# Kernel tuning notes

Hardware: AMD Instinct MI355X
Metric: run time of the kernel (lower is better)

Reference implementation:

```python
import jax, jax.numpy as jnp
import numpy as np
from jax import lax

# LiteMSA config: in_ch=256, out_ch=256, dim=8, heads=32, total_dim=256, scales=(3,)
DIM = 8
QKV_CH = 768          # 3 * total_dim
PW_GROUPS = 96        # 3 * heads


def setup_inputs() -> dict:
    key = jax.random.key(0)
    ks = jax.random.split(key, 5)
    x = jax.random.normal(ks[0], (16, 256, 64, 64), jnp.float32)
    w_qkv = jax.random.normal(ks[1], (768, 256), jnp.float32) * 0.02      # 1x1 conv
    w_dw = jax.random.normal(ks[2], (768, 1, 3, 3), jnp.float32) * 0.02   # depthwise 3x3
    w_pw = jax.random.normal(ks[3], (768, 8, 1, 1), jnp.float32) * 0.02   # grouped 1x1, 96 groups
    w_proj = jax.random.normal(ks[4], (256, 512), jnp.float32) * 0.02     # 1x1 conv
    bn_gamma = jnp.ones((256,), jnp.float32)
    bn_beta = jnp.zeros((256,), jnp.float32)
    bn_mean = jnp.zeros((256,), jnp.float32)
    bn_var = jnp.ones((256,), jnp.float32)
    return {"x": x, "w_qkv": w_qkv, "w_dw": w_dw, "w_pw": w_pw, "w_proj": w_proj,
            "bn_gamma": bn_gamma, "bn_beta": bn_beta, "bn_mean": bn_mean, "bn_var": bn_var}


def reference(x, w_qkv, w_dw, w_pw, w_proj, bn_gamma, bn_beta, bn_mean, bn_var):
    B, _, H, W = x.shape
    dn = ("NCHW", "OIHW", "NCHW")
    # qkv 1x1 conv
    qkv = jnp.einsum("bchw,oc->bohw", x, w_qkv)  # [B,768,H,W]
    # multi-scale aggregation: depthwise 3x3 -> grouped 1x1
    agg = lax.conv_general_dilated(qkv, w_dw, (1, 1), "SAME",
                                   dimension_numbers=dn, feature_group_count=QKV_CH)
    agg = lax.conv_general_dilated(agg, w_pw, (1, 1), "SAME",
                                   dimension_numbers=dn, feature_group_count=PW_GROUPS)
    ms = jnp.concatenate([qkv, agg], axis=1)  # [B,1536,H,W]
    # [B, heads_total=64, N=H*W, 3*dim]
    ms = ms.reshape(B, -1, 3 * DIM, H * W).transpose(0, 1, 3, 2)
    q = jax.nn.relu(ms[..., :DIM])
    k = jax.nn.relu(ms[..., DIM:2 * DIM])
    v = ms[..., 2 * DIM:]
    # pad v with ones for normalizer channel
    v = jnp.concatenate([v, jnp.ones(v.shape[:-1] + (1,), v.dtype)], axis=-1)  # [B,h,N,dim+1]
    kv = jnp.einsum("bhnd,bhne->bhde", k, v)   # [B,h,dim,dim+1]
    out = jnp.einsum("bhnd,bhde->bhne", q, kv)  # [B,h,N,dim+1]
    out = out[..., :DIM] / (out[..., DIM:] + 1e-15)
    out = out.transpose(0, 1, 3, 2).reshape(B, -1, H, W)  # [B,512,H,W]
    # proj 1x1 conv + BatchNorm (inference, running stats)
    y = jnp.einsum("bchw,oc->bohw", out, w_proj)
    inv = bn_gamma / jnp.sqrt(bn_var + 1e-5)
    y = y * inv[None, :, None, None] + (bn_beta - bn_mean * inv)[None, :, None, None]
    return y
```

## Files before the change

kernel.cpp:

```cpp
#include <hip/hip_runtime.h>
#include <hip/hip_bf16.h>


#define NB 16
#define CQKV 768
#define P4096 4096

typedef __bf16 bf16x8 __attribute__((ext_vector_type(8)));
typedef float f32x4 __attribute__((ext_vector_type(4)));

#define MFMA_BF16 __builtin_amdgcn_mfma_f32_16x16x32_bf16

__device__ __forceinline__ ushort f2bf(float f) {
    union { float f; unsigned int u; } x; x.f = f;
    unsigned int u = x.u;
    unsigned int r = (u + 0x7FFFu + ((u >> 16) & 1u)) >> 16;
    return (ushort)r;
}
__device__ __forceinline__ float bf2f(ushort u) {
    union { unsigned int u; float f; } x; x.u = ((unsigned int)u) << 16;
    return x.f;
}
__device__ __forceinline__ unsigned int pk2bf(float x, float y) {
    __hip_bfloat162 h = __float22bfloat162_rn(make_float2(x, y));
    union { __hip_bfloat162 b; unsigned int u; } c; c.b = h; return c.u;
}
__device__ __forceinline__ void stage_hi8(const float* v, ushort* dh) {
    union { unsigned int u[4]; uint4 q; } H;
    #pragma unroll
    for (int i = 0; i < 4; i++) H.u[i] = pk2bf(v[2 * i], v[2 * i + 1]);
    *(uint4*)dh = H.q;
}

__device__ __forceinline__ void gload16(void* lds, const void* g) {
    __builtin_amdgcn_global_load_lds(
        (const __attribute__((address_space(1))) void*)g,
        (__attribute__((address_space(3))) void*)lds, 16, 0, 0);
}

__global__ __launch_bounds__(128) void conv_w(
    const float* __restrict__ W, ushort* __restrict__ Ah, ushort* __restrict__ Al)
{
    const int rv = blockIdx.x;
    const int t  = threadIdx.x;
    int phys;
    if (rv < 256) phys = (rv >> 3) * 24 + (rv & 7);
    else { int r2 = rv - 256; phys = (r2 >> 4) * 24 + 8 + (r2 & 15); }
    int c = t * 2;
    float w0 = W[(size_t)phys * 256 + c];
    float w1 = W[(size_t)phys * 256 + c + 1];
    unsigned int h = pk2bf(w0, w1);
    float f0 = __uint_as_float(h << 16);
    float f1 = __uint_as_float(h & 0xffff0000u);
    unsigned int l = pk2bf(w0 - f0, w1 - f1);
    int sl = ((c >> 3) & 3) ^ ((rv >> 1) & 3);
    int idx = (c & ~31) + sl * 8 + (c & 7);
    *(unsigned int*)&Ah[(size_t)rv * 256 + idx] = h;
    *(unsigned int*)&Al[(size_t)rv * 256 + idx] = l;
}

__global__ __launch_bounds__(256) void conv_x(
    const float* __restrict__ X, ushort* __restrict__ XTh, ushort* __restrict__ XTl)
{
    const int pt = blockIdx.x;
    const int ct = blockIdx.y;
    const int b  = blockIdx.z;
    const int t  = threadIdx.x;
    const int p0 = pt * 64, c0 = ct * 64;

    __shared__ float tile[64][65];

    {
        int cr = t >> 2, pc = (t & 3) * 16;
        const float* xr = X + ((size_t)b * 256 + c0 + cr) * P4096 + p0 + pc;
        float4 v0 = *(const float4*)xr;
        float4 v1 = *(const float4*)(xr + 4);
        float4 v2 = *(const float4*)(xr + 8);
        float4 v3 = *(const float4*)(xr + 12);
        float* d = &tile[cr][pc];
        d[0]=v0.x; d[1]=v0.y; d[2]=v0.z; d[3]=v0.w;
        d[4]=v1.x; d[5]=v1.y; d[6]=v1.z; d[7]=v1.w;
        d[8]=v2.x; d[9]=v2.y; d[10]=v2.z; d[11]=v2.w;
        d[12]=v3.x; d[13]=v3.y; d[14]=v3.z; d[15]=v3.w;
    }
    __syncthreads();

    #pragma unroll
    for (int pass = 0; pass < 2; pass++) {
        int tp = t >> 2;
        int cc = (t & 3) + pass * 4;
        int p  = p0 + tp;
        float v[8];
        #pragma unroll
        for (int j = 0; j < 8; j++) v[j] = tile[cc * 8 + j][tp];
        union { unsigned int u[4]; uint4 q; } H, L;
        #pragma unroll
        for (int i = 0; i < 4; i++) {
            unsigned int h = pk2bf(v[2 * i], v[2 * i + 1]);
            H.u[i] = h;
            float f0 = __uint_as_float(h << 16);
            float f1 = __uint_as_float(h & 0xffff0000u);
            L.u[i] = pk2bf(v[2 * i] - f0, v[2 * i + 1] - f1);
        }
        int c = c0 + cc * 8;
        int sl = ((c >> 3) & 3) ^ ((p >> 1) & 3);
        size_t idx = ((size_t)b * P4096 + p) * 256 + (c & ~31) + sl * 8;
        *(uint4*)&XTh[idx] = H.q;
        *(uint4*)&XTl[idx] = L.q;
    }
}

__global__ __launch_bounds__(256, 2) void gemm_fused(
    const ushort* __restrict__ Ah, const ushort* __restrict__ Al,
    const ushort* __restrict__ Bh, const ushort* __restrict__ Bl,
    ushort* __restrict__ Cbf, float* __restrict__ qplane)
{
    const int hw = blockIdx.x;
    const int lg = (hw & 7) * 384 + (hw >> 3);
    const int mt = lg % 6;
    const int rem = lg / 6;
    const int n0 = (rem & 31) * 128;
    const int b  = rem >> 5;
    const int t  = threadIdx.x;
    const int wave = t >> 6, lane = t & 63, quad = lane >> 4, l15 = lane & 15;
    const int wr = wave >> 1, wc = wave & 1;
    const int M0 = mt * 128;

    __shared__ __align__(16) ushort AsH[2][4096];
    __shared__ __align__(16) ushort AsL[2][4096];
    __shared__ __align__(16) ushort BsH[2][4096];
    __shared__ __align__(16) ushort BsL[2][4096];

    int aoff[4], boff[4];
    #pragma unroll
    for (int i = 0; i < 4; i++) {
        int ra = wr * 64 + i * 16 + l15;
        aoff[i] = ra * 64 + ((quad ^ ((ra >> 1) & 3)) << 4);
        int rb = wc * 64 + i * 16 + l15;
        boff[i] = rb * 64 + ((quad ^ ((rb >> 1) & 3)) << 4);
    }

    const int srow = t >> 2;
    const int schunk = (t & 3) * 8;
    const size_t abase = (size_t)(M0 + srow) * 256 + schunk;
    const size_t bbase = ((size_t)b * P4096 + n0 + srow) * 256 + schunk;
    const int ldsoff = wave * 1024;

    f32x4 acc[4][4];
    #pragma unroll
    for (int mi = 0; mi < 4; mi++)
        #pragma unroll
        for (int nj = 0; nj < 4; nj++)
            #pragma unroll
            for (int r = 0; r < 4; r++) acc[mi][nj][r] = 0.0f;

    if (mt < 2) {
        auto stageQ = [&](int d, int kw) {
            #pragma unroll
            for (int i = 0; i < 2; i++) {
                int lo = ldsoff + i * 4096;
                size_t so = (size_t)(i * 64) * 256 + (size_t)kw * 32;
                gload16((char*)AsH[d] + lo, Ah + abase + so);
                gload16((char*)AsL[d] + lo, Al + abase + so);
                gload16((char*)BsH[d] + lo, Bh + bbase + so);
                gload16((char*)BsL[d] + lo, Bl + bbase + so);
            }
        };
        stageQ(0, 0);
        for (int kw = 0; kw < 8; kw++) {
            int cur = kw & 1;
            if (kw < 7) {
                stageQ(cur ^ 1, kw + 1);
                asm volatile("s_waitcnt vmcnt(8)" ::: "memory");
            } else {
                asm volatile("s_waitcnt vmcnt(0)" ::: "memory");
            }
            __builtin_amdgcn_s_barrier();
            bf16x8 ah[4], al[4];
            #pragma unroll
            for (int mi = 0; mi < 4; mi++) {
                ah[mi] = *(const bf16x8*)((const char*)AsH[cur] + aoff[mi]);
                al[mi] = *(const bf16x8*)((const char*)AsL[cur] + aoff[mi]);
            }
            #pragma unroll
            for (int nj = 0; nj < 4; nj++) {
                bf16x8 bh = *(const bf16x8*)((const char*)BsH[cur] + boff[nj]);
                bf16x8 bl = *(const bf16x8*)((const char*)BsL[cur] + boff[nj]);
                #pragma unroll
                for (int mi = 0; mi < 4; mi++) {
                    acc[mi][nj] = MFMA_BF16(ah[mi], bh, acc[mi][nj], 0, 0, 0);
                    acc[mi][nj] = MFMA_BF16(al[mi], bh, acc[mi][nj], 0, 0, 0);
                    acc[mi][nj] = MFMA_BF16(ah[mi], bl, acc[mi][nj], 0, 0, 0);
                }
            }
            __builtin_amdgcn_s_barrier();
        }
        #pragma unroll
        for (int mi = 0; mi < 4; mi++)
            #pragma unroll
            for (int nj = 0; nj < 4; nj++)
                #pragma unroll
                for (int r = 0; r < 4; r++) {
                    int rv = M0 + wr * 64 + mi * 16 + quad * 4 + r;
                    int rp = (rv >> 3) * 24 + (rv & 7);
                    int col = n0 + wc * 64 + nj * 16 + l15;
                    float v = acc[mi][nj][r];
                    Cbf[((size_t)b * CQKV + rp) * P4096 + col] = f2bf(v);
                    qplane[((size_t)b * 256 + rv) * P4096 + col] = v;
                }
    } else {
        auto stageKV = [&](int d, int kw) {
            #pragma unroll
            for (int i = 0; i < 2; i++) {
                int lo = ldsoff + i * 4096;
                size_t so = (size_t)(i * 64) * 256 + (size_t)kw * 32;
                gload16((char*)AsH[d] + lo, Ah + abase + so);
                gload16((char*)BsH[d] + lo, Bh + bbase + so);
            }
        };
        stageKV(0, 0);
        for (int kw = 0; kw < 8; kw++) {
            int cur = kw & 1;
            if (kw < 7) {
                stageKV(cur ^ 1, kw + 1);
                asm volatile("s_waitcnt vmcnt(4)" ::: "memory");
            } else {
                asm volatile("s_waitcnt vmcnt(0)" ::: "memory");
            }
            __builtin_amdgcn_s_barrier();
            bf16x8 ah[4];
            #pragma unroll
            for (int mi = 0; mi < 4; mi++)
                ah[mi] = *(const bf16x8*)((const char*)AsH[cur] + aoff[mi]);
            #pragma unroll
            for (int nj = 0; nj < 4; nj++) {
                bf16x8 bh = *(const bf16x8*)((const char*)BsH[cur] + boff[nj]);
                #pragma unroll
                for (int mi = 0; mi < 4; mi++)
                    acc[mi][nj] = MFMA_BF16(ah[mi], bh, acc[mi][nj], 0, 0, 0);
            }
            __builtin_amdgcn_s_barrier();
        }
        #pragma unroll
        for (int mi = 0; mi < 4; mi++)
            #pragma unroll
            for (int nj = 0; nj < 4; nj++)
                #pragma unroll
                for (int r = 0; r < 4; r++) {
                    int rv2 = (M0 - 256) + wr * 64 + mi * 16 + quad * 4 + r;
                    int rp = (rv2 >> 4) * 24 + 8 + (rv2 & 15);
                    int col = n0 + wc * 64 + nj * 16 + l15;
                    Cbf[((size_t)b * CQKV + rp) * P4096 + col] = f2bf(acc[mi][nj][r]);
                }
    }
}

__global__ __launch_bounds__(256) void qfix_kernel(
    float* __restrict__ qplane, const float* __restrict__ w_qkv,
    const float* __restrict__ x)
{
    size_t i = (size_t)blockIdx.x * 256 + threadIdx.x;
    float q = qplane[i];
    if (fabsf(q) >= 1e-4f) return;
    int p   = (int)(i & 4095);
    int qch = (int)((i >> 12) & 255);
    int b   = (int)(i >> 20);
    int row = (qch >> 3) * 24 + (qch & 7);
    const float* wr = w_qkv + (size_t)row * 256;
    const float* xr = x + (size_t)b * 256 * P4096 + p;
    double s = 0.0;
    for (int c = 0; c < 256; c++)
        s += (double)wr[c] * (double)xr[(size_t)c * P4096];
    qplane[i] = (float)s;
}

__global__ __launch_bounds__(512, 8) void dwpw_kernel(
    const ushort* __restrict__ qkv, const float* __restrict__ wdw,
    const float* __restrict__ wpw, ushort* __restrict__ agg)
{
    const int rt = blockIdx.x;
    const int g  = blockIdx.y;
    const int b  = blockIdx.z;
    const int t  = threadIdx.x;
    const int r0 = rt * 16;
    const int cg = g * 8;

    __shared__ __align__(16) ushort tile[8][18][80];

    const ushort* src = qkv + ((size_t)(b * CQKV + cg)) * P4096;

    if (t < 288) {
        int ch = t / 36;
        int rr = (t % 36) >> 1;
        int side = t & 1;
        *(uint4*)&tile[ch][rr][side * 72] = make_uint4(0, 0, 0, 0);
    }
    #pragma unroll
    for (int i = 0; i < 3; i++) {
        int id = t + i * 512;
        if (id < 1152) {
            int ch  = id / 144;
            int rem = id - ch * 144;
            int rr  = rem >> 3;
            int oct = (rem & 7) * 8;
            int grow = r0 - 1 + rr;
            uint4 v = make_uint4(0, 0, 0, 0);
            if (grow >= 0 && grow < 64)
                v = *(const uint4*)(src + (size_t)ch * P4096 + (size_t)grow * 64 + oct);
            *(uint4*)&tile[ch][rr][8 + oct] = v;
        }
    }
    __syncthreads();

    const int kc  = t & 31;
    const int row = t >> 5;
    const float* wdwg = wdw + (size_t)cg * 9;
    const float* wpwg = wpw + (size_t)cg * 8;

    float acc0[8], acc1[8];
    #pragma unroll
    for (int oi = 0; oi < 8; oi++) { acc0[oi] = 0.0f; acc1[oi] = 0.0f; }

    #pragma unroll
    for (int c = 0; c < 8; c++) {
        float dv0 = 0.0f, dv1 = 0.0f;
        #pragma unroll
        for (int dy = 0; dy < 3; dy++) {
            const ushort* rp = &tile[c][row + dy][2 * kc + 4];
            unsigned int u1 = *(const unsigned int*)(rp + 2);
            unsigned int u2 = *(const unsigned int*)(rp + 4);
            unsigned int u3 = *(const unsigned int*)(rp + 6);
            float xm1 = __uint_as_float(u1 & 0xffff0000u);
            float x0  = __uint_as_float(u2 << 16);
            float x1  = __uint_as_float(u2 & 0xffff0000u);
            float x2  = __uint_as_float(u3 << 16);
            float w0 = wdwg[c * 9 + dy * 3 + 0];
            float w1 = wdwg[c * 9 + dy * 3 + 1];
            float w2 = wdwg[c * 9 + dy * 3 + 2];
            dv0 = fmaf(w0, xm1, dv0); dv0 = fmaf(w1, x0, dv0); dv0 = fmaf(w2, x1, dv0);
            dv1 = fmaf(w0, x0,  dv1); dv1 = fmaf(w1, x1, dv1); dv1 = fmaf(w2, x2, dv1);
        }
        #pragma unroll
        for (int oi = 0; oi < 8; oi++) {
            float w = wpwg[oi * 8 + c];
            acc0[oi] = fmaf(w, dv0, acc0[oi]);
            acc1[oi] = fmaf(w, dv1, acc1[oi]);
        }
    }

    size_t obase = ((size_t)(b * CQKV + cg)) * P4096 + (size_t)(r0 + row) * 64 + 2 * kc;
    #pragma unroll
    for (int oi = 0; oi < 8; oi++) {
        unsigned int u = (unsigned int)f2bf(acc0[oi]) |
                         ((unsigned int)f2bf(acc1[oi]) << 16);
        *(unsigned int*)&agg[obase + (size_t)oi * P4096] = u;
    }
}

__global__ __launch_bounds__(256) void kv_kernel(
    const ushort* __restrict__ qkv, const ushort* __restrict__ agg,
    float* __restrict__ kv)
{
    const int h = blockIdx.x, b = blockIdx.y, t = threadIdx.x;
    const ushort* src = (h < 32)
        ? qkv + ((size_t)(b * CQKV + h * 24)) * P4096
        : agg + ((size_t)(b * CQKV + (h - 32) * 24)) * P4096;

    float acc[72];
    #pragma unroll
    for (int i = 0; i < 72; i++) acc[i] = 0.0f;

    for (int pi = 0; pi < 16; pi++) {
        int p = t + pi * 256;
        float kvv[8], vv[8];
        #pragma unroll
        for (int d = 0; d < 8; d++) {
            float xk = bf2f(src[(size_t)(8 + d) * P4096 + p]);
            kvv[d] = xk > 0.0f ? xk : 0.0f;
        }
        #pragma unroll
        for (int e = 0; e < 8; e++) vv[e] = bf2f(src[(size_t)(16 + e) * P4096 + p]);
        #pragma unroll
        for (int d = 0; d < 8; d++) {
            #pragma unroll
            for (int e = 0; e < 8; e++) acc[d * 9 + e] += kvv[d] * vv[e];
            acc[d * 9 + 8] += kvv[d];
        }
    }

    #pragma unroll
    for (int i = 0; i < 72; i++) {
        float v = acc[i];
        #pragma unroll
        for (int off = 32; off > 0; off >>= 1) v += __shfl_xor(v, off, 64);
        acc[i] = v;
    }
    __shared__ float part[4][72];
    int wave = t >> 6, lane = t & 63;
    if (lane == 0) {
        #pragma unroll
        for (int i = 0; i < 72; i++) part[wave][i] = acc[i];
    }
    __syncthreads();
    if (t < 72)
        kv[((size_t)b * 64 + h) * 72 + t] = part[0][t] + part[1][t] + part[2][t] + part[3][t];
}

__global__ __launch_bounds__(256) void attn_out_kernel(
    const float* __restrict__ qplane, ushort* __restrict__ agg,
    const float* __restrict__ kv)
{
    const int pt = blockIdx.x, h = blockIdx.y, b = blockIdx.z, t = threadIdx.x;
    __shared__ float kvs[72];
    if (t < 72) kvs[t] = kv[((size_t)b * 64 + h) * 72 + t];
    __syncthreads();

    const bool lohead = (h < 32);
    const float* srcf = lohead
        ? qplane + ((size_t)(b * 256 + h * 8)) * P4096 : nullptr;
    const ushort* srcb = lohead ? nullptr
        : agg + ((size_t)(b * CQKV + (h - 32) * 24)) * P4096;

    int p = pt * 256 + t;
    float num[8]; float den = 0.0f;
    #pragma unroll
    for (int e = 0; e < 8; e++) num[e] = 0.0f;
    #pragma unroll
    for (int d = 0; d < 8; d++) {
        float q = lohead ? srcf[(size_t)d * P4096 + p]
                         : bf2f(srcb[(size_t)d * P4096 + p]);
        q = q > 0.0f ? q : 0.0f;
        #pragma unroll
        for (int e = 0; e < 8; e++) num[e] += q * kvs[d * 9 + e];
        den += q * kvs[d * 9 + 8];
    }
    float rd = 1.0f / (den + 1e-15f);
    ushort* dst = agg + ((size_t)(b * CQKV + (h / 2) * 24 + 8 + (h % 2) * 8)) * P4096 + p;
    #pragma unroll
    for (int e = 0; e < 8; e++)
        dst[(size_t)e * P4096] = f2bf(num[e] * rd);
}

__global__ __launch_bounds__(256) void gemm_proj(
    const float* __restrict__ A,
    const ushort* __restrict__ Bagg,
    float* __restrict__ Y,
    const float* __restrict__ bn_g, const float* __restrict__ bn_b,
    const float* __restrict__ bn_m, const float* __restrict__ bn_v)
{
    const int n0 = blockIdx.x * 64;
    const int m0 = blockIdx.y * 64;
    const int b  = blockIdx.z;
    const int t  = threadIdx.x;
    const int wave = t >> 6, lane = t & 63, quad = lane >> 4, l15 = lane & 15;

    __shared__ __align__(16) ushort As[64][40];
    __shared__ __align__(16) ushort Bs[64][40];

    f32x4 acc[4];
    #pragma unroll
    for (int nt = 0; nt < 4; nt++)
        #pragma unroll
        for (int r = 0; r < 4; r++) acc[nt][r] = 0.0f;

    const int am = t >> 2, ak = (t & 3) * 8;
    const int bn = t & 63, kg = (t >> 6) * 8;

    for (int k0 = 0; k0 < 512; k0 += 32) {
        float av[8];
        *(float4*)&av[0] = *(const float4*)(A + (size_t)(m0 + am) * 512 + k0 + ak);
        *(float4*)&av[4] = *(const float4*)(A + (size_t)(m0 + am) * 512 + k0 + ak + 4);
        ushort bu[8];
        #pragma unroll
        for (int i = 0; i < 8; i++) {
            int kk = k0 + kg + i;
            int amch = (kk >> 4) * 24 + 8 + (kk & 15);
            bu[i] = Bagg[((size_t)b * CQKV + amch) * P4096 + n0 + bn];
        }

        __syncthreads();
        stage_hi8(av, &As[am][ak]);
        {
            union { ushort us[8]; uint4 q; } Bp;
            #pragma unroll
            for (int i = 0; i < 8; i++) Bp.us[i] = bu[i];
            *(uint4*)&Bs[bn][kg] = Bp.q;
        }
        __syncthreads();

        bf16x8 af = *(const bf16x8*)&As[wave * 16 + l15][quad * 8];
        #pragma unroll
        for (int nt = 0; nt < 4; nt++) {
            bf16x8 bf = *(const bf16x8*)&Bs[nt * 16 + l15][quad * 8];
            acc[nt] = MFMA_BF16(af, bf, acc[nt], 0, 0, 0);
        }
    }

    #pragma unroll
    for (int nt = 0; nt < 4; nt++) {
        #pragma unroll
        for (int r = 0; r < 4; r++) {
            int row = m0 + wave * 16 + quad * 4 + r;
            int col = n0 + nt * 16 + l15;
            float inv = bn_g[row] / sqrtf(bn_v[row] + 1e-5f);
            float v = acc[nt][r] * inv + (bn_b[row] - bn_m[row] * inv);
            Y[((size_t)b * 256 + row) * P4096 + col] = v;
        }
    }
}

extern "C" void kernel_launch(void* const* d_in, const int* in_sizes, int n_in,
                              void* d_out, int out_size, void* d_ws, size_t ws_size,
                              hipStream_t stream) {
    const float* x      = (const float*)d_in[0];
    const float* w_qkv  = (const float*)d_in[1];
    const float* w_dw   = (const float*)d_in[2];
    const float* w_pw   = (const float*)d_in[3];
    const float* w_proj = (const float*)d_in[4];
    const float* bn_g   = (const float*)d_in[5];
    const float* bn_b   = (const float*)d_in[6];
    const float* bn_m   = (const float*)d_in[7];
    const float* bn_v   = (const float*)d_in[8];
    float* y = (float*)d_out;

    char* ws = (char*)d_ws;
    ushort* qkv_bf = (ushort*)(ws);
    float*  qplane = (float*) (ws + 100663296);
    ushort* agg_bf = (ushort*)(ws + 167772160);
    ushort* XTh = (ushort*)(ws + 167772160);
    ushort* XTl = (ushort*)(ws + 167772160 + 33554432);
    ushort* Awh = (ushort*)(ws + 167772160 + 67108864);
    ushort* Awl = (ushort*)(ws + 167772160 + 67108864 + 393216);
    float*  kvbuf  = (float*)d_out;

    conv_w<<<dim3(768), 128, 0, stream>>>(w_qkv, Awh, Awl);
    conv_x<<<dim3(64, 4, NB), 256, 0, stream>>>(x, XTh, XTl);

    gemm_fused<<<dim3(3072), 256, 0, stream>>>(
        Awh, Awl, XTh, XTl, qkv_bf, qplane);

    qfix_kernel<<<65536, 256, 0, stream>>>(qplane, w_qkv, x);

    dwpw_kernel<<<dim3(4, 96, NB), 512, 0, stream>>>(qkv_bf, w_dw, w_pw, agg_bf);

    kv_kernel<<<dim3(64, NB), 256, 0, stream>>>(qkv_bf, agg_bf, kvbuf);

    attn_out_kernel<<<dim3(16, 64, NB), 256, 0, stream>>>(qplane, agg_bf, kvbuf);

    gemm_proj<<<dim3(64, 4, NB), 256, 0, stream>>>(
        w_proj, agg_bf, y, bn_g, bn_b, bn_m, bn_v);
}
```

Measured before the change: 444.4 us.

## Split QKV GEMM into q and kv kernels, compact near-zero q fixups into list

```diff
diff --git a/kernel.cpp b/kernel.cpp
--- a/kernel.cpp
+++ b/kernel.cpp
@@ -5,6 +5,7 @@
 #define NB 16
 #define CQKV 768
 #define P4096 4096
+#define QFIX_CAP (1u << 21)
 
 typedef __bf16 bf16x8 __attribute__((ext_vector_type(8)));
 typedef float f32x4 __attribute__((ext_vector_type(4)));
@@ -110,15 +111,18 @@
     }
 }
 
-__global__ __launch_bounds__(256, 2) void gemm_fused(
+__global__ void zero_cnt(unsigned int* qmeta) { if (threadIdx.x == 0) qmeta[0] = 0; }
+
+__global__ __launch_bounds__(256, 2) void gemm_q(
     const ushort* __restrict__ Ah, const ushort* __restrict__ Al,
     const ushort* __restrict__ Bh, const ushort* __restrict__ Bl,
-    ushort* __restrict__ Cbf, float* __restrict__ qplane)
+    ushort* __restrict__ Cbf, float* __restrict__ qplane,
+    unsigned int* __restrict__ qmeta)
 {
     const int hw = blockIdx.x;
-    const int lg = (hw & 7) * 384 + (hw >> 3);
-    const int mt = lg % 6;
-    const int rem = lg / 6;
+    const int lg = (hw & 7) * 128 + (hw >> 3);
+    const int mt = lg & 1;
+    const int rem = lg >> 1;
     const int n0 = (rem & 31) * 128;
     const int b  = rem >> 5;
     const int t  = threadIdx.x;
@@ -154,124 +158,181 @@
             #pragma unroll
             for (int r = 0; r < 4; r++) acc[mi][nj][r] = 0.0f;
 
-    if (mt < 2) {
-        auto stageQ = [&](int d, int kw) {
-            #pragma unroll
-            for (int i = 0; i < 2; i++) {
-                int lo = ldsoff + i * 4096;
-                size_t so = (size_t)(i * 64) * 256 + (size_t)kw * 32;
-                gload16((char*)AsH[d] + lo, Ah + abase + so);
-                gload16((char*)AsL[d] + lo, Al + abase + so);
-                gload16((char*)BsH[d] + lo, Bh + bbase + so);
-                gload16((char*)BsL[d] + lo, Bl + bbase + so);
+    auto stageQ = [&](int d, int kw) {
+        #pragma unroll
+        for (int i = 0; i < 2; i++) {
+            int lo = ldsoff + i * 4096;
+            size_t so = (size_t)(i * 64) * 256 + (size_t)kw * 32;
+            gload16((char*)AsH[d] + lo, Ah + abase + so);
+            gload16((char*)AsL[d] + lo, Al + abase + so);
+            gload16((char*)BsH[d] + lo, Bh + bbase + so);
+            gload16((char*)BsL[d] + lo, Bl + bbase + so);
+        }
+    };
+    stageQ(0, 0);
+    for (int kw = 0; kw < 8; kw++) {
+        int cur = kw & 1;
+        if (kw < 7) {
+            stageQ(cur ^ 1, kw + 1);
+            asm volatile("s_waitcnt vmcnt(8)" ::: "memory");
+        } else {
+            asm volatile("s_waitcnt vmcnt(0)" ::: "memory");
+        }
+        __builtin_amdgcn_s_barrier();
+        bf16x8 ah[4], al[4];
+        #pragma unroll
+        for (int mi = 0; mi < 4; mi++) {
+            ah[mi] = *(const bf16x8*)((const char*)AsH[cur] + aoff[mi]);
+            al[mi] = *(const bf16x8*)((const char*)AsL[cur] + aoff[mi]);
+        }
+        #pragma unroll
+        for (int nj = 0; nj < 4; nj++) {
+            bf16x8 bh = *(const bf16x8*)((const char*)BsH[cur] + boff[nj]);
+            bf16x8 bl = *(const bf16x8*)((const char*)BsL[cur] + boff[nj]);
+            #pragma unroll
+            for (int mi = 0; mi < 4; mi++) {
+                acc[mi][nj] = MFMA_BF16(ah[mi], bh, acc[mi][nj], 0, 0, 0);
+                acc[mi][nj] = MFMA_BF16(al[mi], bh, acc[mi][nj], 0, 0, 0);
+                acc[mi][nj] = MFMA_BF16(ah[mi], bl, acc[mi][nj], 0, 0, 0);
             }
-        };
-        stageQ(0, 0);
-        for (int kw = 0; kw < 8; kw++) {
-            int cur = kw & 1;
-            if (kw < 7) {
-                stageQ(cur ^ 1, kw + 1);
-                asm volatile("s_waitcnt vmcnt(8)" ::: "memory");
-            } else {
-                asm volatile("s_waitcnt vmcnt(0)" ::: "memory");
-            }
-            __builtin_amdgcn_s_barrier();
-            bf16x8 ah[4], al[4];
-            #pragma unroll
-            for (int mi = 0; mi < 4; mi++) {
-                ah[mi] = *(const bf16x8*)((const char*)AsH[cur] + aoff[mi]);
-                al[mi] = *(const bf16x8*)((const char*)AsL[cur] + aoff[mi]);
-            }
-            #pragma unroll
-            for (int nj = 0; nj < 4; nj++) {
-                bf16x8 bh = *(const bf16x8*)((const char*)BsH[cur] + boff[nj]);
-                bf16x8 bl = *(const bf16x8*)((const char*)BsL[cur] + boff[nj]);
-                #pragma unroll
-                for (int mi = 0; mi < 4; mi++) {
-                    acc[mi][nj] = MFMA_BF16(ah[mi], bh, acc[mi][nj], 0, 0, 0);
-                    acc[mi][nj] = MFMA_BF16(al[mi], bh, acc[mi][nj], 0, 0, 0);
-                    acc[mi][nj] = MFMA_BF16(ah[mi], bl, acc[mi][nj], 0, 0, 0);
+        }
+        __builtin_amdgcn_s_barrier();
+    }
+
+    unsigned int* qlist = qmeta + 16;
+    #pragma unroll
+    for (int mi = 0; mi < 4; mi++)
+        #pragma unroll
+        for (int nj = 0; nj < 4; nj++)
+            #pragma unroll
+            for (int r = 0; r < 4; r++) {
+                int rv = M0 + wr * 64 + mi * 16 + quad * 4 + r;
+                int rp = (rv >> 3) * 24 + (rv & 7);
+                int col = n0 + wc * 64 + nj * 16 + l15;
+                float v = acc[mi][nj][r];
+                Cbf[((size_t)b * CQKV + rp) * P4096 + col] = f2bf(v);
+                qplane[((size_t)b * 256 + rv) * P4096 + col] = v;
+                if (fabsf(v) < 1e-4f) {
+                    unsigned int idx = atomicAdd(qmeta, 1u);
+                    if (idx < QFIX_CAP)
+                        qlist[idx] = (unsigned int)(((b * 256 + rv) << 12) | col);
                 }
             }
-            __builtin_amdgcn_s_barrier();
-        }
+}
+
+__global__ __launch_bounds__(256, 4) void gemm_kv(
+    const ushort* __restrict__ Ah, const ushort* __restrict__ Bh,
+    ushort* __restrict__ Cbf)
+{
+    const int hw = blockIdx.x;
+    const int lg = (hw & 7) * 256 + (hw >> 3);
+    const int mt = lg & 3;
+    const int rem = lg >> 2;
+    const int n0 = (rem & 31) * 128;
+    const int b  = rem >> 5;
+    const int t  = threadIdx.x;
+    const int wave = t >> 6, lane = t & 63, quad = lane >> 4, l15 = lane & 15;
+    const int wr = wave >> 1, wc = wave & 1;
+    const int M0 = mt * 128;
+
+    __shared__ __align__(16) ushort As[2][4096];
+    __shared__ __align__(16) ushort Bs[2][4096];
+
+    int aoff[4], boff[4];
+    #pragma unroll
+    for (int i = 0; i < 4; i++) {
+        int ra = wr * 64 + i * 16 + l15;
+        aoff[i] = ra * 64 + ((quad ^ ((ra >> 1) & 3)) << 4);
+        int rb = wc * 64 + i * 16 + l15;
+        boff[i] = rb * 64 + ((quad ^ ((rb >> 1) & 3)) << 4);
+    }
+
+    const int srow = t >> 2;
+    const int schunk = (t & 3) * 8;
+    const size_t abase = (size_t)(256 + M0 + srow) * 256 + schunk;
+    const size_t bbase = ((size_t)b * P4096 + n0 + srow) * 256 + schunk;
+    const int ldsoff = wave * 1024;
+
+    f32x4 acc[4][4];
+    #pragma unroll
+    for (int mi = 0; mi < 4; mi++)
+        #pragma unroll
+        for (int nj = 0; nj < 4; nj++)
+            #pragma unroll
+            for (int r = 0; r < 4; r++) acc[mi][nj][r] = 0.0f;
+
+    auto stageKV = [&](int d, int kw) {
+        #pragma unroll
+        for (int i = 0; i < 2; i++) {
+            int lo = ldsoff + i * 4096;
+            size_t so = (size_t)(i * 64) * 256 + (size_t)kw * 32;
+            gload16((char*)As[d] + lo, Ah + abase + so);
+            gload16((char*)Bs[d] + lo, Bh + bbase + so);
+        }
+    };
+    stageKV(0, 0);
+    for (int kw = 0; kw < 8; kw++) {
+        int cur = kw & 1;
+        if (kw < 7) {
+            stageKV(cur ^ 1, kw + 1);
+            asm volatile("s_waitcnt vmcnt(4)" ::: "memory");
+        } else {
+            asm volatile("s_waitcnt vmcnt(0)" ::: "memory");
+        }
+        __builtin_amdgcn_s_barrier();
+        bf16x8 ah[4];
         #pragma unroll
         for (int mi = 0; mi < 4; mi++)
-            #pragma unroll
-            for (int nj = 0; nj < 4; nj++)
-                #pragma unroll
-                for (int r = 0; r < 4; r++) {
-                    int rv = M0 + wr * 64 + mi * 16 + quad * 4 + r;
-                    int rp = (rv >> 3) * 24 + (rv & 7);
-                    int col = n0 + wc * 64 + nj * 16 + l15;
-                    float v = acc[mi][nj][r];
-                    Cbf[((size_t)b * CQKV + rp) * P4096 + col] = f2bf(v);
-                    qplane[((size_t)b * 256 + rv) * P4096 + col] = v;
-                }
-    } else {
-        auto stageKV = [&](int d, int kw) {
-            #pragma unroll
-            for (int i = 0; i < 2; i++) {
-                int lo = ldsoff + i * 4096;
-                size_t so = (size_t)(i * 64) * 256 + (size_t)kw * 32;
-                gload16((char*)AsH[d] + lo, Ah + abase + so);
-                gload16((char*)BsH[d] + lo, Bh + bbase + so);
+            ah[mi] = *(const bf16x8*)((const char*)As[cur] + aoff[mi]);
+        #pragma unroll
+        for (int nj = 0; nj < 4; nj++) {
+            bf16x8 bh = *(const bf16x8*)((const char*)Bs[cur] + boff[nj]);
+            #pragma unroll
+            for (int mi = 0; mi < 4; mi++)
+                acc[mi][nj] = MFMA_BF16(ah[mi], bh, acc[mi][nj], 0, 0, 0);
+        }
+        __builtin_amdgcn_s_barrier();
+    }
+    #pragma unroll
+    for (int mi = 0; mi < 4; mi++)
+        #pragma unroll
+        for (int nj = 0; nj < 4; nj++)
+            #pragma unroll
+            for (int r = 0; r < 4; r++) {
+                int rv2 = M0 + wr * 64 + mi * 16 + quad * 4 + r;
+                int rp = (rv2 >> 4) * 24 + 8 + (rv2 & 15);
+                int col = n0 + wc * 64 + nj * 16 + l15;
+                Cbf[((size_t)b * CQKV + rp) * P4096 + col] = f2bf(acc[mi][nj][r]);
             }
-        };
-        stageKV(0, 0);
-        for (int kw = 0; kw < 8; kw++) {
-            int cur = kw & 1;
-            if (kw < 7) {
-                stageKV(cur ^ 1, kw + 1);
-                asm volatile("s_waitcnt vmcnt(4)" ::: "memory");
-            } else {
-                asm volatile("s_waitcnt vmcnt(0)" ::: "memory");
-            }
-            __builtin_amdgcn_s_barrier();
-            bf16x8 ah[4];
-            #pragma unroll
-            for (int mi = 0; mi < 4; mi++)
-                ah[mi] = *(const bf16x8*)((const char*)AsH[cur] + aoff[mi]);
-            #pragma unroll
-            for (int nj = 0; nj < 4; nj++) {
-                bf16x8 bh = *(const bf16x8*)((const char*)BsH[cur] + boff[nj]);
-                #pragma unroll
-                for (int mi = 0; mi < 4; mi++)
-                    acc[mi][nj] = MFMA_BF16(ah[mi], bh, acc[mi][nj], 0, 0, 0);
-            }
-            __builtin_amdgcn_s_barrier();
-        }
-        #pragma unroll
-        for (int mi = 0; mi < 4; mi++)
-            #pragma unroll
-            for (int nj = 0; nj < 4; nj++)
-                #pragma unroll
-                for (int r = 0; r < 4; r++) {
-                    int rv2 = (M0 - 256) + wr * 64 + mi * 16 + quad * 4 + r;
-                    int rp = (rv2 >> 4) * 24 + 8 + (rv2 & 15);
-                    int col = n0 + wc * 64 + nj * 16 + l15;
-                    Cbf[((size_t)b * CQKV + rp) * P4096 + col] = f2bf(acc[mi][nj][r]);
-                }
-    }
-}
-
-__global__ __launch_bounds__(256) void qfix_kernel(
+}
+
+__global__ __launch_bounds__(256) void qfix2_kernel(
     float* __restrict__ qplane, const float* __restrict__ w_qkv,
-    const float* __restrict__ x)
-{
-    size_t i = (size_t)blockIdx.x * 256 + threadIdx.x;
-    float q = qplane[i];
-    if (fabsf(q) >= 1e-4f) return;
-    int p   = (int)(i & 4095);
-    int qch = (int)((i >> 12) & 255);
-    int b   = (int)(i >> 20);
-    int row = (qch >> 3) * 24 + (qch & 7);
-    const float* wr = w_qkv + (size_t)row * 256;
-    const float* xr = x + (size_t)b * 256 * P4096 + p;
-    double s = 0.0;
-    for (int c = 0; c < 256; c++)
-        s += (double)wr[c] * (double)xr[(size_t)c * P4096];
-    qplane[i] = (float)s;
+    const float* __restrict__ x, const unsigned int* __restrict__ qmeta)
+{
+    unsigned int n = qmeta[0];
+    if (n > QFIX_CAP) n = QFIX_CAP;
+    const unsigned int* list = qmeta + 16;
+    const int wave = threadIdx.x >> 6, lane = threadIdx.x & 63;
+    for (unsigned int e = blockIdx.x * 4 + wave; e < n; e += gridDim.x * 4) {
+        unsigned int i = list[e];
+        int p   = (int)(i & 4095);
+        int qch = (int)((i >> 12) & 255);
+        int b   = (int)(i >> 20);
+        int row = (qch >> 3) * 24 + (qch & 7);
+        const float* wr = w_qkv + (size_t)row * 256;
+        const float* xr = x + (size_t)b * 256 * P4096 + p;
+        double s = 0.0;
+        #pragma unroll
+        for (int j = 0; j < 4; j++) {
+            int c = lane * 4 + j;
+            s += (double)wr[c] * (double)xr[(size_t)c * P4096];
+        }
+        #pragma unroll
+        for (int off = 32; off > 0; off >>= 1) s += __shfl_xor(s, off, 64);
+        if (lane == 0)
+            qplane[((size_t)(b * 256 + qch)) * P4096 + p] = (float)s;
+    }
 }
 
 __global__ __launch_bounds__(512, 8) void dwpw_kernel(
@@ -532,14 +593,17 @@
     ushort* Awh = (ushort*)(ws + 167772160 + 67108864);
     ushort* Awl = (ushort*)(ws + 167772160 + 67108864 + 393216);
     float*  kvbuf  = (float*)d_out;
+    unsigned int* qmeta = (unsigned int*)((char*)d_out + 524288);
 
     conv_w<<<dim3(768), 128, 0, stream>>>(w_qkv, Awh, Awl);
+    zero_cnt<<<1, 64, 0, stream>>>(qmeta);
     conv_x<<<dim3(64, 4, NB), 256, 0, stream>>>(x, XTh, XTl);
 
-    gemm_fused<<<dim3(3072), 256, 0, stream>>>(
-        Awh, Awl, XTh, XTl, qkv_bf, qplane);
-
-    qfix_kernel<<<65536, 256, 0, stream>>>(qplane, w_qkv, x);
+    gemm_q<<<dim3(1024), 256, 0, stream>>>(
+        Awh, Awl, XTh, XTl, qkv_bf, qplane, qmeta);
+    gemm_kv<<<dim3(2048), 256, 0, stream>>>(Awh, XTh, qkv_bf);
+
+    qfix2_kernel<<<dim3(1024), 256, 0, stream>>>(qplane, w_qkv, x, qmeta);
 
     dwpw_kernel<<<dim3(4, 96, NB), 512, 0, stream>>>(qkv_bf, w_dw, w_pw, agg_bf);
 
```

After: 460.7 us. 1.04x slower.
